# Optimization experiments

Hardware: AMD Instinct MI355X
Metric: run time of the kernel (lower is better)

The kernel has to match this reference:

```python
import jax, jax.numpy as jnp
import numpy as np

BETA = 0.5
LAMBDA = 0.5
EPS = 1e-24


def setup_inputs() -> dict:
    key = jax.random.key(0)
    k1, k2 = jax.random.split(key)
    seq = jax.random.normal(k1, (32, 512, 128), dtype=jnp.float32)
    fism_items = jax.random.normal(k2, (32, 2048, 128), dtype=jnp.float32)
    return {"seq": seq, "fism_items": fism_items}


def reference(seq, fism_items):
    # scores: [B, L, N]
    w = jnp.einsum('bld,bnd->bln', seq, fism_items)
    w_shift = w - jnp.max(w, axis=-1, keepdims=True)
    exp_w = jnp.exp(w_shift)
    exp_sum = jnp.sum(exp_w, axis=-1, keepdims=True)
    if BETA != 1.0:
        exp_sum = jnp.power(exp_sum, jnp.float32(BETA))
    att = exp_w / (exp_sum + EPS)  # power-normalized softmax
    att_vecs = jnp.einsum('bln,bnd->bld', att, fism_items)
    if LAMBDA < 1:
        return seq * (1.0 - LAMBDA) + seq * att_vecs * LAMBDA
    return seq * att_vecs
```

## Files before the change

### kernel.cpp

```cpp
#include <hip/hip_runtime.h>
#include <hip/hip_bf16.h>
#include <math.h>

typedef _Float16 half8  __attribute__((ext_vector_type(8)));
typedef _Float16 half2v __attribute__((ext_vector_type(2)));
typedef __fp16   fp16x2 __attribute__((ext_vector_type(2)));
typedef float    f32x4  __attribute__((ext_vector_type(4)));

#define DDIM 128
#define LQ   512
#define NKV  2048
#define KVB  64
#define NCH  (NKV / KVB)

union U32H2 { unsigned u; fp16x2 h; };
union H8W   { unsigned u[4]; half8 h; };

__device__ __forceinline__ int swzv(int d) { return ((d ^ (d >> 4)) & 7) << 3; }

__global__ __launch_bounds__(256, 1)
void gattn(const float* __restrict__ seq, const float* __restrict__ fism,
           float* __restrict__ out)
{
  const int tid  = threadIdx.x;
  const int lane = tid & 63;
  const int wv   = tid >> 6;
  const int q16  = lane & 15;
  const int g    = lane >> 4;
  const int b    = blockIdx.x >> 3;
  const int qb   = (blockIdx.x & 7) * 64;

  const float* seqB = seq  + (size_t)b * LQ * DDIM;
  const float* fisB = fism + (size_t)b * NKV * DDIM;
  float*       outB = out  + (size_t)b * LQ * DDIM;

  __shared__ _Float16 Ksh[KVB * DDIM];
  __shared__ _Float16 VTsh[DDIM * KVB];

  half8 qf[4];
  {
    const int qrow = qb + wv * 16 + q16;
    #pragma unroll
    for (int c = 0; c < 4; ++c) {
      const float* p = seqB + (size_t)qrow * DDIM + c * 32 + g * 8;
      float4 a  = *(const float4*)p;
      float4 b2 = *(const float4*)(p + 4);
      half8 h;
      h[0]=(_Float16)a.x;  h[1]=(_Float16)a.y;  h[2]=(_Float16)a.z;  h[3]=(_Float16)a.w;
      h[4]=(_Float16)b2.x; h[5]=(_Float16)b2.y; h[6]=(_Float16)b2.z; h[7]=(_Float16)b2.w;
      qf[c] = h;
    }
  }

  const int sp   = tid >> 3;
  const int dgrp = tid & 7;

  f32x4 acc[8];
  #pragma unroll
  for (int i = 0; i < 8; ++i) { f32x4 z = {0.f,0.f,0.f,0.f}; acc[i] = z; }

  float m_run = -INFINITY, tmax = -INFINITY, S_run = 0.f;

  auto write_stage = [&](const float4* v) {
    #pragma unroll
    for (int r = 0; r < 2; ++r) {
      const int row = 2*sp + r;
      #pragma unroll
      for (int hh = 0; hh < 2; ++hh) {
        const float4 x = v[r*4 + hh*2];
        const float4 y = v[r*4 + hh*2 + 1];
        half8 h;
        h[0]=(_Float16)x.x; h[1]=(_Float16)x.y; h[2]=(_Float16)x.z; h[3]=(_Float16)x.w;
        h[4]=(_Float16)y.x; h[5]=(_Float16)y.y; h[6]=(_Float16)y.z; h[7]=(_Float16)y.w;
        const int idx = row*DDIM + ((dgrp*16 + hh*8) ^ ((row & 7) << 3));
        *(half8*)&Ksh[idx] = h;
      }
    }
    #pragma unroll
    for (int k = 0; k < 16; ++k) {
      const int d = dgrp*16 + k;
      half2v pk;
      pk[0] = (_Float16)(((const float*)&v[k>>2])[k&3]);
      pk[1] = (_Float16)(((const float*)&v[4 + (k>>2)])[k&3]);
      const int idx = d*KVB + ((2*sp) ^ swzv(d));
      *(half2v*)&VTsh[idx] = pk;
    }
  };

  {
    float4 stg[8];
    #pragma unroll
    for (int r = 0; r < 2; ++r)
      #pragma unroll
      for (int k = 0; k < 4; ++k)
        stg[r*4+k] = *(const float4*)(fisB + (size_t)(2*sp + r)*DDIM + dgrp*16 + k*4);
    write_stage(stg);
  }

  for (int t = 0; t < NCH; ++t) {
    float4 nxt[8];
    const bool have = (t + 1 < NCH);
    if (have) {
      const float* src = fisB + (size_t)(t+1)*KVB*DDIM;
      #pragma unroll
      for (int r = 0; r < 2; ++r)
        #pragma unroll
        for (int k = 0; k < 4; ++k)
          nxt[r*4+k] = *(const float4*)(src + (size_t)(2*sp + r)*DDIM + dgrp*16 + k*4);
    }
    __syncthreads();

    f32x4 sv[4];
    #pragma unroll
    for (int ns = 0; ns < 4; ++ns) {
      f32x4 x = {0.f,0.f,0.f,0.f};
      const int row = ns*16 + q16;
      #pragma unroll
      for (int c = 0; c < 4; ++c) {
        const int idx = row*DDIM + ((c*32 + g*8) ^ ((row & 7) << 3));
        half8 kf = *(const half8*)&Ksh[idx];
        x = __builtin_amdgcn_mfma_f32_16x16x32_f16(kf, qf[c], x, 0, 0, 0);
      }
      sv[ns] = x;
    }

    float cmax = sv[0][0];
    #pragma unroll
    for (int ns = 0; ns < 4; ++ns)
      #pragma unroll
      for (int i = 0; i < 4; ++i)
        cmax = fmaxf(cmax, sv[ns][i]);
    cmax = fmaxf(cmax, __shfl_xor(cmax, 16));
    cmax = fmaxf(cmax, __shfl_xor(cmax, 32));
    tmax = fmaxf(tmax, cmax);
    if (__any(cmax > m_run + 8.f)) {
      const float mn = fmaxf(m_run, cmax);
      const float sc = __expf(m_run - mn);
      S_run *= sc;
      m_run = mn;
      const float s0 = __shfl(sc, (g<<4) | (4*g + 0));
      const float s1 = __shfl(sc, (g<<4) | (4*g + 1));
      const float s2 = __shfl(sc, (g<<4) | (4*g + 2));
      const float s3 = __shfl(sc, (g<<4) | (4*g + 3));
      const f32x4 scv = {s0, s1, s2, s3};
      #pragma unroll
      for (int dsu = 0; dsu < 8; ++dsu) acc[dsu] *= scv;
    }
    float lsum = 0.f;
    #pragma unroll
    for (int ns = 0; ns < 4; ++ns)
      #pragma unroll
      for (int i = 0; i < 4; ++i) {
        const float p = __expf(sv[ns][i] - m_run);
        sv[ns][i] = p;
        lsum += p;
      }
    lsum += __shfl_xor(lsum, 16);
    lsum += __shfl_xor(lsum, 32);
    S_run += lsum;

    unsigned upk[4][2];
    #pragma unroll
    for (int ns = 0; ns < 4; ++ns) {
      U32H2 u0, u1;
      u0.h = __builtin_amdgcn_cvt_pkrtz(sv[ns][0], sv[ns][1]);
      u1.h = __builtin_amdgcn_cvt_pkrtz(sv[ns][2], sv[ns][3]);
      upk[ns][0] = u0.u; upk[ns][1] = u1.u;
    }
    #pragma unroll
    for (int c = 0; c < 2; ++c) {
      H8W aw;
      #pragma unroll
      for (int tt = 0; tt < 4; ++tt) {
        const int src = q16 + 16 * ((g & 1) * 2 + (tt >> 1));
        const unsigned lo = (unsigned)__shfl((int)upk[2*c  ][tt & 1], src);
        const unsigned hi = (unsigned)__shfl((int)upk[2*c+1][tt & 1], src);
        aw.u[tt] = (g < 2) ? lo : hi;
      }
      const half8 pa = aw.h;
      #pragma unroll
      for (int dsu = 0; dsu < 8; ++dsu) {
        const int d = dsu*16 + q16;
        const int idx = d*KVB + ((c*32 + g*8) ^ swzv(d));
        half8 vf = *(const half8*)&VTsh[idx];
        acc[dsu] = __builtin_amdgcn_mfma_f32_16x16x32_f16(pa, vf, acc[dsu], 0, 0, 0);
      }
    }

    __syncthreads();
    if (have) write_stage(nxt);
  }

  const float fs = __expf(0.5f * (m_run - tmax)) / sqrtf(S_run);
  float fsr[4];
  #pragma unroll
  for (int i = 0; i < 4; ++i)
    fsr[i] = __shfl(fs, (g<<4) | (4*g + i));
  #pragma unroll
  for (int dsu = 0; dsu < 8; ++dsu) {
    #pragma unroll
    for (int i = 0; i < 4; ++i) {
      const int qrow = qb + wv*16 + 4*g + i;
      const int d = dsu*16 + q16;
      const float s = seqB[(size_t)qrow * DDIM + d];
      outB[(size_t)qrow * DDIM + d] = 0.5f * s * (1.f + acc[dsu][i] * fsr[i]);
    }
  }
}

extern "C" void kernel_launch(void* const* d_in, const int* in_sizes, int n_in,
                              void* d_out, int out_size, void* d_ws, size_t ws_size,
                              hipStream_t stream) {
  const float* seq  = (const float*)d_in[0];
  const float* fism = (const float*)d_in[1];
  float* out = (float*)d_out;
  gattn<<<dim3(256), dim3(256), 0, stream>>>(seq, fism, out);
}
```

Measured before the change: 64.45 us.

## Split KV sequence across two wave groups per block and merge softmax states

Doubles the block to 512 threads so two groups of four waves each process alternating 64-row KV chunks, with a pair of chunks staged per iteration into double LDS buffers. At the end, the second group writes its accumulators and running max/sum stats to shared memory, and the first group merges them with the power-normalized scaling before writing output. Block indices are also swizzled so that consecutive blocks map to different batches. This raises per-CU wave count and halves the serial loop length. The cost is an extra LDS reduction step and higher LDS/register pressure under launch_bounds(512,2).

```diff
diff --git a/kernel.cpp b/kernel.cpp
--- a/kernel.cpp
+++ b/kernel.cpp
@@ -11,35 +11,40 @@
 #define LQ   512
 #define NKV  2048
 #define KVB  64
-#define NCH  (NKV / KVB)
+#define NPAIR (NKV / (2 * KVB))
 
 union U32H2 { unsigned u; fp16x2 h; };
 union H8W   { unsigned u[4]; half8 h; };
 
 __device__ __forceinline__ int swzv(int d) { return ((d ^ (d >> 4)) & 7) << 3; }
 
-__global__ __launch_bounds__(256, 1)
+__global__ __launch_bounds__(512, 2)
 void gattn(const float* __restrict__ seq, const float* __restrict__ fism,
            float* __restrict__ out)
 {
   const int tid  = threadIdx.x;
   const int lane = tid & 63;
   const int wv   = tid >> 6;
+  const int half = wv >> 2;
+  const int wq   = wv & 3;
   const int q16  = lane & 15;
   const int g    = lane >> 4;
-  const int b    = blockIdx.x >> 3;
-  const int qb   = (blockIdx.x & 7) * 64;
+
+  const int swz = (blockIdx.x & 7) * 32 + (blockIdx.x >> 3);
+  const int b   = swz >> 3;
+  const int qb  = (swz & 7) * 64;
 
   const float* seqB = seq  + (size_t)b * LQ * DDIM;
   const float* fisB = fism + (size_t)b * NKV * DDIM;
   float*       outB = out  + (size_t)b * LQ * DDIM;
 
-  __shared__ _Float16 Ksh[KVB * DDIM];
-  __shared__ _Float16 VTsh[DDIM * KVB];
+  __shared__ _Float16 Ksh[2][KVB * DDIM];
+  __shared__ _Float16 VTsh[2][DDIM * KVB];
+  __shared__ float    stats[4][16][3];
 
   half8 qf[4];
   {
-    const int qrow = qb + wv * 16 + q16;
+    const int qrow = qb + wq * 16 + q16;
     #pragma unroll
     for (int c = 0; c < 4; ++c) {
       const float* p = seqB + (size_t)qrow * DDIM + c * 32 + g * 8;
@@ -54,6 +59,8 @@
 
   const int sp   = tid >> 3;
   const int dgrp = tid & 7;
+  const int bsel = sp >> 5;
+  const int spc  = sp & 31;
 
   f32x4 acc[8];
   #pragma unroll
@@ -64,7 +71,7 @@
   auto write_stage = [&](const float4* v) {
     #pragma unroll
     for (int r = 0; r < 2; ++r) {
-      const int row = 2*sp + r;
+      const int row = 2*spc + r;
       #pragma unroll
       for (int hh = 0; hh < 2; ++hh) {
         const float4 x = v[r*4 + hh*2];
@@ -73,7 +80,7 @@
         h[0]=(_Float16)x.x; h[1]=(_Float16)x.y; h[2]=(_Float16)x.z; h[3]=(_Float16)x.w;
         h[4]=(_Float16)y.x; h[5]=(_Float16)y.y; h[6]=(_Float16)y.z; h[7]=(_Float16)y.w;
         const int idx = row*DDIM + ((dgrp*16 + hh*8) ^ ((row & 7) << 3));
-        *(half8*)&Ksh[idx] = h;
+        *(half8*)&Ksh[bsel][idx] = h;
       }
     }
     #pragma unroll
@@ -82,8 +89,8 @@
       half2v pk;
       pk[0] = (_Float16)(((const float*)&v[k>>2])[k&3]);
       pk[1] = (_Float16)(((const float*)&v[4 + (k>>2)])[k&3]);
-      const int idx = d*KVB + ((2*sp) ^ swzv(d));
-      *(half2v*)&VTsh[idx] = pk;
+      const int idx = d*KVB + ((2*spc) ^ swzv(d));
+      *(half2v*)&VTsh[bsel][idx] = pk;
     }
   };
 
@@ -97,11 +104,11 @@
     write_stage(stg);
   }
 
-  for (int t = 0; t < NCH; ++t) {
+  for (int tp = 0; tp < NPAIR; ++tp) {
     float4 nxt[8];
-    const bool have = (t + 1 < NCH);
+    const bool have = (tp + 1 < NPAIR);
     if (have) {
-      const float* src = fisB + (size_t)(t+1)*KVB*DDIM;
+      const float* src = fisB + (size_t)(tp+1)*2*KVB*DDIM;
       #pragma unroll
       for (int r = 0; r < 2; ++r)
         #pragma unroll
@@ -118,7 +125,7 @@
       #pragma unroll
       for (int c = 0; c < 4; ++c) {
         const int idx = row*DDIM + ((c*32 + g*8) ^ ((row & 7) << 3));
-        half8 kf = *(const half8*)&Ksh[idx];
+        half8 kf = *(const half8*)&Ksh[half][idx];
         x = __builtin_amdgcn_mfma_f32_16x16x32_f16(kf, qf[c], x, 0, 0, 0);
       }
       sv[ns] = x;
@@ -182,7 +189,7 @@
       for (int dsu = 0; dsu < 8; ++dsu) {
         const int d = dsu*16 + q16;
         const int idx = d*KVB + ((c*32 + g*8) ^ swzv(d));
-        half8 vf = *(const half8*)&VTsh[idx];
+        half8 vf = *(const half8*)&VTsh[half][idx];
         acc[dsu] = __builtin_amdgcn_mfma_f32_16x16x32_f16(pa, vf, acc[dsu], 0, 0, 0);
       }
     }
@@ -191,19 +198,54 @@
     if (have) write_stage(nxt);
   }
 
-  const float fs = __expf(0.5f * (m_run - tmax)) / sqrtf(S_run);
-  float fsr[4];
-  #pragma unroll
-  for (int i = 0; i < 4; ++i)
-    fsr[i] = __shfl(fs, (g<<4) | (4*g + i));
-  #pragma unroll
-  for (int dsu = 0; dsu < 8; ++dsu) {
+  if (half == 1) {
+    float* d0 = (float*)&Ksh[1][0];
+    float* d1 = (float*)&VTsh[1][0];
+    const int base = (wq*64 + lane) * 16;
+    #pragma unroll
+    for (int dsu = 0; dsu < 4; ++dsu) {
+      *(f32x4*)&d0[base + dsu*4] = acc[dsu];
+      *(f32x4*)&d1[base + dsu*4] = acc[dsu + 4];
+    }
+    if (g == 0) {
+      stats[wq][q16][0] = m_run;
+      stats[wq][q16][1] = S_run;
+      stats[wq][q16][2] = tmax;
+    }
+  }
+  __syncthreads();
+
+  if (half == 0) {
+    const float m1 = stats[wq][q16][0];
+    const float S1 = stats[wq][q16][1];
+    const float t1 = stats[wq][q16][2];
+    const float M  = fmaxf(tmax, t1);
+    const float a0 = __expf(m_run - M);
+    const float a1 = __expf(m1 - M);
+    const float rs = rsqrtf(a0 * S_run + a1 * S1);
+    const float f0 = a0 * rs, f1 = a1 * rs;
+    float f0r[4], f1r[4];
     #pragma unroll
     for (int i = 0; i < 4; ++i) {
-      const int qrow = qb + wv*16 + 4*g + i;
-      const int d = dsu*16 + q16;
-      const float s = seqB[(size_t)qrow * DDIM + d];
-      outB[(size_t)qrow * DDIM + d] = 0.5f * s * (1.f + acc[dsu][i] * fsr[i]);
+      const int src = (g<<4) | (4*g + i);
+      f0r[i] = __shfl(f0, src);
+      f1r[i] = __shfl(f1, src);
+    }
+    const float* d0 = (const float*)&Ksh[1][0];
+    const float* d1 = (const float*)&VTsh[1][0];
+    const int base = (wq*64 + lane) * 16;
+    #pragma unroll
+    for (int dsu = 0; dsu < 8; ++dsu) {
+      const f32x4 a1v = (dsu < 4) ? *(const f32x4*)&d0[base + dsu*4]
+                                  : *(const f32x4*)&d1[base + (dsu-4)*4];
+      #pragma unroll
+      for (int i = 0; i < 4; ++i) {
+        const int qrow = qb + wq*16 + 4*g + i;
+        const int d = dsu*16 + q16;
+        const float s = seqB[(size_t)qrow * DDIM + d];
+        const float av = acc[dsu][i] * f0r[i] + a1v[i] * f1r[i];
+        outB[(size_t)qrow * DDIM + d] = 0.5f * s * (1.f + av);
+      }
     }
   }
 }
@@ -214,5 +256,5 @@
   const float* seq  = (const float*)d_in[0];
   const float* fism = (const float*)d_in[1];
   float* out = (float*)d_out;
-  gattn<<<dim3(256), dim3(256), 0, stream>>>(seq, fism, out);
+  gattn<<<dim3(256), dim3(512), 0, stream>>>(seq, fism, out);
 }
```

Result: faster. 51.89 us (-19.5%).

## Split KV range across warps with split-K softmax merge and larger grid

Applied to the files above, without the earlier changes.

Each block now handles 32 query rows with 8 waves: 2 query groups by 4 KV quarters. Each wave pair streams its own quarter of the keys in 32-row chunks through a private shared-memory stage. Partial accumulators and softmax stats are merged through shared memory at the end, and block indices are swizzled across batches. This raises the grid from 256 to 512 blocks of 512 threads to fill more CUs and shortens each serial KV loop. The cost is an extra reduction pass through LDS and duplicated Q loads.

```diff
diff --git a/kernel.cpp b/kernel.cpp
--- a/kernel.cpp
+++ b/kernel.cpp
@@ -10,36 +10,42 @@
 #define DDIM 128
 #define LQ   512
 #define NKV  2048
-#define KVB  64
-#define NCH  (NKV / KVB)
+#define KVB  32
+#define NIT  16
 
 union U32H2 { unsigned u; fp16x2 h; };
 union H8W   { unsigned u[4]; half8 h; };
 
-__device__ __forceinline__ int swzv(int d) { return ((d ^ (d >> 4)) & 7) << 3; }
-
-__global__ __launch_bounds__(256, 1)
+__device__ __forceinline__ int swzk(int row) { return (row & 7) << 3; }
+__device__ __forceinline__ int swzv(int d)   { return ((d ^ (d >> 4)) & 3) << 3; }
+
+__global__ __launch_bounds__(512, 4)
 void gattn(const float* __restrict__ seq, const float* __restrict__ fism,
            float* __restrict__ out)
 {
   const int tid  = threadIdx.x;
   const int lane = tid & 63;
   const int wv   = tid >> 6;
+  const int wq   = wv & 1;
+  const int kvq  = wv >> 1;
   const int q16  = lane & 15;
   const int g    = lane >> 4;
-  const int b    = blockIdx.x >> 3;
-  const int qb   = (blockIdx.x & 7) * 64;
+
+  const int swz = (blockIdx.x & 7) * 64 + (blockIdx.x >> 3);
+  const int b   = swz >> 4;
+  const int qb  = (swz & 15) * 32;
 
   const float* seqB = seq  + (size_t)b * LQ * DDIM;
   const float* fisB = fism + (size_t)b * NKV * DDIM;
   float*       outB = out  + (size_t)b * LQ * DDIM;
 
-  __shared__ _Float16 Ksh[KVB * DDIM];
-  __shared__ _Float16 VTsh[DDIM * KVB];
+  __shared__ _Float16 Ksh[4][KVB * DDIM];
+  __shared__ _Float16 VTsh[4][DDIM * KVB];
+  __shared__ float    stats[4][2][16][3];
 
   half8 qf[4];
   {
-    const int qrow = qb + wv * 16 + q16;
+    const int qrow = qb + wq * 16 + q16;
     #pragma unroll
     for (int c = 0; c < 4; ++c) {
       const float* p = seqB + (size_t)qrow * DDIM + c * 32 + g * 8;
@@ -54,6 +60,8 @@
 
   const int sp   = tid >> 3;
   const int dgrp = tid & 7;
+  const int qstg = sp >> 4;
+  const int spc  = sp & 15;
 
   f32x4 acc[8];
   #pragma unroll
@@ -64,7 +72,7 @@
   auto write_stage = [&](const float4* v) {
     #pragma unroll
     for (int r = 0; r < 2; ++r) {
-      const int row = 2*sp + r;
+      const int row = 2*spc + r;
       #pragma unroll
       for (int hh = 0; hh < 2; ++hh) {
         const float4 x = v[r*4 + hh*2];
@@ -72,8 +80,8 @@
         half8 h;
         h[0]=(_Float16)x.x; h[1]=(_Float16)x.y; h[2]=(_Float16)x.z; h[3]=(_Float16)x.w;
         h[4]=(_Float16)y.x; h[5]=(_Float16)y.y; h[6]=(_Float16)y.z; h[7]=(_Float16)y.w;
-        const int idx = row*DDIM + ((dgrp*16 + hh*8) ^ ((row & 7) << 3));
-        *(half8*)&Ksh[idx] = h;
+        const int idx = row*DDIM + ((dgrp*16 + hh*8) ^ swzk(row));
+        *(half8*)&Ksh[qstg][idx] = h;
       }
     }
     #pragma unroll
@@ -82,43 +90,41 @@
       half2v pk;
       pk[0] = (_Float16)(((const float*)&v[k>>2])[k&3]);
       pk[1] = (_Float16)(((const float*)&v[4 + (k>>2)])[k&3]);
-      const int idx = d*KVB + ((2*sp) ^ swzv(d));
-      *(half2v*)&VTsh[idx] = pk;
-    }
+      const int idx = d*KVB + ((2*spc) ^ swzv(d));
+      *(half2v*)&VTsh[qstg][idx] = pk;
+    }
+  };
+
+  auto load_glb = [&](float4* v, int t) {
+    const float* src = fisB + (size_t)(qstg*(NKV/4) + t*KVB) * DDIM;
+    #pragma unroll
+    for (int r = 0; r < 2; ++r)
+      #pragma unroll
+      for (int k = 0; k < 4; ++k)
+        v[r*4+k] = *(const float4*)(src + (size_t)(2*spc + r)*DDIM + dgrp*16 + k*4);
   };
 
   {
     float4 stg[8];
-    #pragma unroll
-    for (int r = 0; r < 2; ++r)
-      #pragma unroll
-      for (int k = 0; k < 4; ++k)
-        stg[r*4+k] = *(const float4*)(fisB + (size_t)(2*sp + r)*DDIM + dgrp*16 + k*4);
+    load_glb(stg, 0);
     write_stage(stg);
   }
 
-  for (int t = 0; t < NCH; ++t) {
+  for (int t = 0; t < NIT; ++t) {
+    __syncthreads();
     float4 nxt[8];
-    const bool have = (t + 1 < NCH);
-    if (have) {
-      const float* src = fisB + (size_t)(t+1)*KVB*DDIM;
-      #pragma unroll
-      for (int r = 0; r < 2; ++r)
-        #pragma unroll
-        for (int k = 0; k < 4; ++k)
-          nxt[r*4+k] = *(const float4*)(src + (size_t)(2*sp + r)*DDIM + dgrp*16 + k*4);
-    }
-    __syncthreads();
-
-    f32x4 sv[4];
-    #pragma unroll
-    for (int ns = 0; ns < 4; ++ns) {
+    const bool have = (t + 1 < NIT);
+    if (have) load_glb(nxt, t + 1);
+
+    f32x4 sv[2];
+    #pragma unroll
+    for (int ns = 0; ns < 2; ++ns) {
       f32x4 x = {0.f,0.f,0.f,0.f};
       const int row = ns*16 + q16;
       #pragma unroll
       for (int c = 0; c < 4; ++c) {
-        const int idx = row*DDIM + ((c*32 + g*8) ^ ((row & 7) << 3));
-        half8 kf = *(const half8*)&Ksh[idx];
+        const int idx = row*DDIM + ((c*32 + g*8) ^ swzk(row));
+        half8 kf = *(const half8*)&Ksh[kvq][idx];
         x = __builtin_amdgcn_mfma_f32_16x16x32_f16(kf, qf[c], x, 0, 0, 0);
       }
       sv[ns] = x;
@@ -126,7 +132,7 @@
 
     float cmax = sv[0][0];
     #pragma unroll
-    for (int ns = 0; ns < 4; ++ns)
+    for (int ns = 0; ns < 2; ++ns)
       #pragma unroll
       for (int i = 0; i < 4; ++i)
         cmax = fmaxf(cmax, sv[ns][i]);
@@ -148,7 +154,7 @@
     }
     float lsum = 0.f;
     #pragma unroll
-    for (int ns = 0; ns < 4; ++ns)
+    for (int ns = 0; ns < 2; ++ns)
       #pragma unroll
       for (int i = 0; i < 4; ++i) {
         const float p = __expf(sv[ns][i] - m_run);
@@ -159,30 +165,29 @@
     lsum += __shfl_xor(lsum, 32);
     S_run += lsum;
 
-    unsigned upk[4][2];
-    #pragma unroll
-    for (int ns = 0; ns < 4; ++ns) {
+    unsigned upk[2][2];
+    #pragma unroll
+    for (int ns = 0; ns < 2; ++ns) {
       U32H2 u0, u1;
       u0.h = __builtin_amdgcn_cvt_pkrtz(sv[ns][0], sv[ns][1]);
       u1.h = __builtin_amdgcn_cvt_pkrtz(sv[ns][2], sv[ns][3]);
       upk[ns][0] = u0.u; upk[ns][1] = u1.u;
     }
-    #pragma unroll
-    for (int c = 0; c < 2; ++c) {
+    {
       H8W aw;
       #pragma unroll
       for (int tt = 0; tt < 4; ++tt) {
         const int src = q16 + 16 * ((g & 1) * 2 + (tt >> 1));
-        const unsigned lo = (unsigned)__shfl((int)upk[2*c  ][tt & 1], src);
-        const unsigned hi = (unsigned)__shfl((int)upk[2*c+1][tt & 1], src);
+        const unsigned lo = (unsigned)__shfl((int)upk[0][tt & 1], src);
+        const unsigned hi = (unsigned)__shfl((int)upk[1][tt & 1], src);
         aw.u[tt] = (g < 2) ? lo : hi;
       }
       const half8 pa = aw.h;
       #pragma unroll
       for (int dsu = 0; dsu < 8; ++dsu) {
         const int d = dsu*16 + q16;
-        const int idx = d*KVB + ((c*32 + g*8) ^ swzv(d));
-        half8 vf = *(const half8*)&VTsh[idx];
+        const int idx = d*KVB + ((g*8) ^ swzv(d));
+        half8 vf = *(const half8*)&VTsh[kvq][idx];
         acc[dsu] = __builtin_amdgcn_mfma_f32_16x16x32_f16(pa, vf, acc[dsu], 0, 0, 0);
       }
     }
@@ -191,19 +196,64 @@
     if (have) write_stage(nxt);
   }
 
-  const float fs = __expf(0.5f * (m_run - tmax)) / sqrtf(S_run);
-  float fsr[4];
-  #pragma unroll
-  for (int i = 0; i < 4; ++i)
-    fsr[i] = __shfl(fs, (g<<4) | (4*g + i));
-  #pragma unroll
-  for (int dsu = 0; dsu < 8; ++dsu) {
-    #pragma unroll
-    for (int i = 0; i < 4; ++i) {
-      const int qrow = qb + wv*16 + 4*g + i;
-      const int d = dsu*16 + q16;
-      const float s = seqB[(size_t)qrow * DDIM + d];
-      outB[(size_t)qrow * DDIM + d] = 0.5f * s * (1.f + acc[dsu][i] * fsr[i]);
+  __syncthreads();
+  if (kvq != 0) {
+    const int rgn = (kvq - 1) * 2 + wq;
+    float* base = (rgn < 4) ? ((float*)&Ksh[0][0]  + rgn * 2048)
+                            : ((float*)&VTsh[0][0] + (rgn - 4) * 2048);
+    float* p = base + lane * 32;
+    #pragma unroll
+    for (int dsu = 0; dsu < 8; ++dsu)
+      *(f32x4*)&p[dsu*4] = acc[dsu];
+    if (g == 0) {
+      stats[kvq][wq][q16][0] = m_run;
+      stats[kvq][wq][q16][1] = S_run;
+      stats[kvq][wq][q16][2] = tmax;
+    }
+  }
+  __syncthreads();
+
+  if (kvq == 0) {
+    float mj[4], Sj[4], tj[4];
+    mj[0] = m_run; Sj[0] = S_run; tj[0] = tmax;
+    #pragma unroll
+    for (int j = 1; j < 4; ++j) {
+      mj[j] = stats[j][wq][q16][0];
+      Sj[j] = stats[j][wq][q16][1];
+      tj[j] = stats[j][wq][q16][2];
+    }
+    const float M = fmaxf(fmaxf(tj[0], tj[1]), fmaxf(tj[2], tj[3]));
+    float aj[4], den = 0.f;
+    #pragma unroll
+    for (int j = 0; j < 4; ++j) { aj[j] = __expf(mj[j] - M); den += aj[j] * Sj[j]; }
+    const float rs = rsqrtf(den);
+    float fr[4][4];
+    #pragma unroll
+    for (int j = 0; j < 4; ++j) {
+      const float fj = aj[j] * rs;
+      #pragma unroll
+      for (int i = 0; i < 4; ++i)
+        fr[j][i] = __shfl(fj, (g<<4) | (4*g + i));
+    }
+    #pragma unroll
+    for (int dsu = 0; dsu < 8; ++dsu) {
+      f32x4 av = acc[dsu];
+      av *= (f32x4){fr[0][0], fr[0][1], fr[0][2], fr[0][3]};
+      #pragma unroll
+      for (int j = 1; j < 4; ++j) {
+        const int rgn = (j - 1) * 2 + wq;
+        const float* base = (rgn < 4) ? ((const float*)&Ksh[0][0]  + rgn * 2048)
+                                      : ((const float*)&VTsh[0][0] + (rgn - 4) * 2048);
+        const f32x4 pj = *(const f32x4*)&base[lane*32 + dsu*4];
+        av += pj * (f32x4){fr[j][0], fr[j][1], fr[j][2], fr[j][3]};
+      }
+      #pragma unroll
+      for (int i = 0; i < 4; ++i) {
+        const int qrow = qb + wq*16 + 4*g + i;
+        const int d = dsu*16 + q16;
+        const float s = seqB[(size_t)qrow * DDIM + d];
+        outB[(size_t)qrow * DDIM + d] = 0.5f * s * (1.f + av[i]);
+      }
     }
   }
 }
@@ -214,5 +264,5 @@
   const float* seq  = (const float*)d_in[0];
   const float* fism = (const float*)d_in[1];
   float* out = (float*)d_out;
-  gattn<<<dim3(256), dim3(256), 0, stream>>>(seq, fism, out);
+  gattn<<<dim3(512), dim3(512), 0, stream>>>(seq, fism, out);
 }
```

Measured after the change: 62.29 us. -3.4%, faster.
